# Kernel tuning notes

Measured on AMD Instinct MI355X. Metric: run time of the kernel, lower is better.

The kernel has to match this reference:

```python
import jax, jax.numpy as jnp
import numpy as np

B, T, L, H = 16, 16, 512, 768


def setup_inputs() -> dict:
    key = jax.random.key(0)
    k1, k2, k3, k4, k5, k6 = jax.random.split(key, 6)
    hn = jax.random.normal(k1, (B, L, H), dtype=jnp.float32)
    decoder_out = jax.random.normal(k2, (B, L, H), dtype=jnp.float32)
    W1 = jax.random.normal(k3, (H, H), dtype=jnp.float32) * (1.0 / np.sqrt(H))
    W2 = jax.random.normal(k4, (H, H), dtype=jnp.float32) * (1.0 / np.sqrt(H))
    V = jax.random.normal(k5, (H,), dtype=jnp.float32) * (1.0 / np.sqrt(H))
    # Ragged, consistent pointer indices: T monotone segment starts per sample,
    # gold boundary Yindex[b,t] in [Xindex[b,t], L).
    step = L // T  # 32
    Xindex = jnp.broadcast_to(jnp.arange(T, dtype=jnp.int64) * step, (B, T))
    offsets = jax.random.randint(k6, (B, T), 0, step, dtype=jnp.int64)
    Yindex = Xindex + offsets
    lens = jnp.full((B,), L, dtype=jnp.int64)
    return {"hn": hn, "decoder_out": decoder_out, "W1": W1, "W2": W2, "V": V,
            "Xindex": Xindex, "Yindex": Yindex, "lens": lens}


def reference(hn, decoder_out, W1, W2, V, Xindex, Yindex, lens):
    # Faithful batched form of training_decoder + pointerLayer:
    #   for each sample i, step j:
    #     en = hn[i, Xindex[i,j]:lens[i]]            (ragged suffix)
    #     dj = decoder_out[i, Yindex[i,j]]           (cur_dj = decoder_out[cur_groundy])
    #     s  = selu(V @ selu(W1 en + W2 dj))
    #     loss += NLL(log_softmax(s), Yindex[i,j]-Xindex[i,j])
    WE = jnp.einsum('blh,gh->blg', hn, W1)                        # [B,L,H]  nnW1(en)
    dj = jnp.take_along_axis(decoder_out, Yindex[:, :, None], axis=1)  # [B,T,H]
    WD = jnp.einsum('bth,gh->btg', dj, W2)                        # [B,T,H]  nnW2(dj)
    act = jax.nn.selu(WE[:, None, :, :] + WD[:, :, None, :])      # [B,T,L,H]
    scores = jax.nn.selu(jnp.einsum('btlh,h->btl', act, V))       # [B,T,L]
    pos = jnp.arange(hn.shape[1])
    mask = (pos[None, None, :] >= Xindex[:, :, None]) & (pos[None, None, :] < lens[:, None, None])
    neg_inf = jnp.finfo(scores.dtype).min
    masked = jnp.where(mask, scores, neg_inf)
    logp = masked - jax.scipy.special.logsumexp(masked, axis=-1, keepdims=True)
    # logits index (Yindex - Xindex) in the sliced array == global index Yindex
    gold = jnp.take_along_axis(logp, Yindex[:, :, None], axis=-1)[..., 0]  # [B,T]
    return -jnp.mean(gold)
```

## Files before the change

### kernel.cpp

```cpp
#include <hip/hip_runtime.h>
#include <hip/hip_bf16.h>
#include <math.h>

#define SELU_SCALE 1.0507009873554805f
#define SELU_ALPHA 1.6732632423543772f

static constexpr int B_ = 16, T_ = 16, L_ = 512, H_ = 768;

typedef __bf16 bf16x8 __attribute__((ext_vector_type(8)));
typedef __bf16 bf16x4 __attribute__((ext_vector_type(4)));
typedef float  f32x4  __attribute__((ext_vector_type(4)));

__device__ __forceinline__ float bf_lo(unsigned u) { return __uint_as_float(u << 16); }
__device__ __forceinline__ float bf_hi(unsigned u) { return __uint_as_float(u & 0xFFFF0000u); }

__device__ __forceinline__ float selu_core(float x) {
    float e = fmaf(__expf(x), SELU_ALPHA, -SELU_ALPHA);
    return x > 0.0f ? x : e;
}

__device__ __forceinline__ bf16x4 cvt4(float4 f) {
    bf16x4 o;
    o.x = (__bf16)f.x; o.y = (__bf16)f.y; o.z = (__bf16)f.z; o.w = (__bf16)f.w;
    return o;
}

__device__ __forceinline__ int xsw(int r) { return (r >> 1) & 3; }

__global__ __launch_bounds__(256) void prep_k(
        const float* __restrict__ w1, const float* __restrict__ w2,
        const float* __restrict__ dec, const int* __restrict__ Yi,
        __bf16* __restrict__ w1b, __bf16* __restrict__ w2b,
        float* __restrict__ djf, float* __restrict__ out) {
    const int NW = H_ * H_ / 4;
    int i = blockIdx.x * 256 + threadIdx.x;
    if (i == 0) out[0] = 0.0f;
    if (i < NW) {
        ((bf16x4*)w1b)[i] = cvt4(((const float4*)w1)[i]);
    } else if (i < 2 * NW) {
        int j = i - NW;
        ((bf16x4*)w2b)[j] = cvt4(((const float4*)w2)[j]);
    } else {
        int j = i - 2 * NW;
        int bt = j / 192, c = j % 192;
        int b = bt >> 4;
        int y = Yi[bt];
        ((float4*)djf)[bt * 192 + c] = ((const float4*)dec)[(b * L_ + y) * 192 + c];
    }
}

__global__ __launch_bounds__(256) void gemm_k(
        const float* __restrict__ hn, const float* __restrict__ djf,
        const __bf16* __restrict__ w1b, const __bf16* __restrict__ w2b,
        __bf16* __restrict__ web, __bf16* __restrict__ wdb) {
    __shared__ __bf16 As[64 * 32];
    __shared__ __bf16 Bs[128 * 32];

    int bx = blockIdx.x;
    const float* Af; const __bf16* Bw; __bf16* C; int m0, n0;
    if (bx < 768) {
        Af = hn;  Bw = w1b; C = web;
        m0 = (bx & 127) * 64; n0 = (bx >> 7) * 128;
    } else {
        bx -= 768;
        Af = djf; Bw = w2b; C = wdb;
        m0 = (bx & 3) * 64;   n0 = (bx >> 2) * 128;
    }

    const int tid = threadIdx.x;
    const int wave = tid >> 6, lane = tid & 63;
    const int wm = (wave >> 1) * 32, wn = (wave & 1) * 64;
    const int lr = lane & 15, q = lane >> 4;

    const int arow = tid >> 2, aseg = tid & 3;
    const float* Ag = Af + (size_t)(m0 + arow) * 768 + aseg * 8;
    bf16x8* AsW = (bf16x8*)&As[arow * 32 + ((aseg ^ xsw(arow)) * 8)];

    const int brow = tid >> 1, bs0 = (tid & 1) * 2;
    const __bf16* Bg = Bw + (size_t)(n0 + brow) * 768 + bs0 * 8;
    uint4* BsW0 = (uint4*)&Bs[brow * 32 + (((bs0)     ^ xsw(brow)) * 8)];
    uint4* BsW1 = (uint4*)&Bs[brow * 32 + (((bs0 + 1) ^ xsw(brow)) * 8)];

    int aoff[2], boff[4];
#pragma unroll
    for (int i = 0; i < 2; ++i) {
        int r = wm + i * 16 + lr;
        aoff[i] = r * 32 + (q ^ xsw(r)) * 8;
    }
#pragma unroll
    for (int j = 0; j < 4; ++j) {
        int r = wn + j * 16 + lr;
        boff[j] = r * 32 + (q ^ xsw(r)) * 8;
    }

    f32x4 acc[2][4] = {};

    float4 pax0 = *(const float4*)(Ag);      float4 pax1 = *(const float4*)(Ag + 4);
    uint4  pbx0 = *(const uint4*)(Bg);       uint4  pbx1 = *(const uint4*)(Bg + 8);
    float4 pay0 = *(const float4*)(Ag + 32); float4 pay1 = *(const float4*)(Ag + 36);
    uint4  pby0 = *(const uint4*)(Bg + 32);  uint4  pby1 = *(const uint4*)(Bg + 40);

#pragma unroll 1
    for (int k0 = 0; k0 < 768; k0 += 64) {
        {
            bf16x8 aw;
            aw[0] = (__bf16)pax0.x; aw[1] = (__bf16)pax0.y;
            aw[2] = (__bf16)pax0.z; aw[3] = (__bf16)pax0.w;
            aw[4] = (__bf16)pax1.x; aw[5] = (__bf16)pax1.y;
            aw[6] = (__bf16)pax1.z; aw[7] = (__bf16)pax1.w;
            *AsW  = aw;
            *BsW0 = pbx0;
            *BsW1 = pbx1;
            asm volatile("s_waitcnt lgkmcnt(0)\n\ts_barrier" ::: "memory");
            if (k0 + 64 < 768) {
                pax0 = *(const float4*)(Ag + k0 + 64);
                pax1 = *(const float4*)(Ag + k0 + 68);
                pbx0 = *(const uint4*)(Bg + k0 + 64);
                pbx1 = *(const uint4*)(Bg + k0 + 72);
            }
            bf16x8 af[2], bfr[4];
#pragma unroll
            for (int i = 0; i < 2; ++i) af[i]  = *(const bf16x8*)&As[aoff[i]];
#pragma unroll
            for (int j = 0; j < 4; ++j) bfr[j] = *(const bf16x8*)&Bs[boff[j]];
#pragma unroll
            for (int i = 0; i < 2; ++i)
#pragma unroll
                for (int j = 0; j < 4; ++j)
                    acc[i][j] = __builtin_amdgcn_mfma_f32_16x16x32_bf16(af[i], bfr[j], acc[i][j], 0, 0, 0);
            asm volatile("s_barrier" ::: "memory");
        }
        {
            bf16x8 aw;
            aw[0] = (__bf16)pay0.x; aw[1] = (__bf16)pay0.y;
            aw[2] = (__bf16)pay0.z; aw[3] = (__bf16)pay0.w;
            aw[4] = (__bf16)pay1.x; aw[5] = (__bf16)pay1.y;
            aw[6] = (__bf16)pay1.z; aw[7] = (__bf16)pay1.w;
            *AsW  = aw;
            *BsW0 = pby0;
            *BsW1 = pby1;
            asm volatile("s_waitcnt lgkmcnt(0)\n\ts_barrier" ::: "memory");
            if (k0 + 96 < 768) {
                pay0 = *(const float4*)(Ag + k0 + 96);
                pay1 = *(const float4*)(Ag + k0 + 100);
                pby0 = *(const uint4*)(Bg + k0 + 96);
                pby1 = *(const uint4*)(Bg + k0 + 104);
            }
            bf16x8 af[2], bfr[4];
#pragma unroll
            for (int i = 0; i < 2; ++i) af[i]  = *(const bf16x8*)&As[aoff[i]];
#pragma unroll
            for (int j = 0; j < 4; ++j) bfr[j] = *(const bf16x8*)&Bs[boff[j]];
#pragma unroll
            for (int i = 0; i < 2; ++i)
#pragma unroll
                for (int j = 0; j < 4; ++j)
                    acc[i][j] = __builtin_amdgcn_mfma_f32_16x16x32_bf16(af[i], bfr[j], acc[i][j], 0, 0, 0);
            asm volatile("s_barrier" ::: "memory");
        }
    }

#pragma unroll
    for (int i = 0; i < 2; ++i)
#pragma unroll
        for (int j = 0; j < 4; ++j)
#pragma unroll
            for (int r = 0; r < 4; ++r) {
                int row = m0 + wm + i * 16 + q * 4 + r;
                int col = n0 + wn + j * 16 + lr;
                C[(size_t)row * 768 + col] = (__bf16)acc[i][j][r];
            }
}

__global__ __launch_bounds__(256) void scores_k(
        const __bf16* __restrict__ web, const __bf16* __restrict__ wdb,
        const float* __restrict__ V, const int* __restrict__ Xi,
        float* __restrict__ scores) {
    __shared__ float    we_s[16][772];
    __shared__ unsigned wd_s[16][388];
    __shared__ float    v_s[768];

    const int b = blockIdx.x, l0 = blockIdx.y * 16;

    for (int c = threadIdx.x; c < 16 * 96; c += 256) {
        int r = c / 96, cc = c % 96;
        uint4 v = *(const uint4*)(web + ((size_t)(b * L_ + l0 + r)) * H_ + cc * 8);
        float4 f0, f1;
        f0.x = bf_lo(v.x); f0.y = bf_hi(v.x); f0.z = bf_lo(v.y); f0.w = bf_hi(v.y);
        f1.x = bf_lo(v.z); f1.y = bf_hi(v.z); f1.z = bf_lo(v.w); f1.w = bf_hi(v.w);
        *(float4*)&we_s[r][cc * 8]     = f0;
        *(float4*)&we_s[r][cc * 8 + 4] = f1;
    }
    for (int c = threadIdx.x; c < 16 * 96; c += 256) {
        int r = c / 96, cc = c % 96;
        *(uint4*)&wd_s[r][cc * 4] = *(const uint4*)(wdb + ((size_t)(b * T_ + r)) * H_ + cc * 8);
    }
    if (threadIdx.x < 192) *(float4*)&v_s[threadIdx.x * 4] = ((const float4*)V)[threadIdx.x];
    __syncthreads();

    const int t = threadIdx.x >> 4;
    const int ls = threadIdx.x & 15;
    const int l = l0 + ls;
    const int X = Xi[b * T_ + t];
    if (!__any(l >= X)) return;

    float a0 = 0.f, a1 = 0.f, a2 = 0.f, a3 = 0.f;
#pragma unroll 4
    for (int h = 0; h < H_; h += 8) {
        float4 w0 = *(const float4*)&we_s[ls][h];
        float4 w1 = *(const float4*)&we_s[ls][h + 4];
        uint4  wd = *(const uint4*)&wd_s[t][h >> 1];
        float4 v0 = *(const float4*)&v_s[h];
        float4 v1 = *(const float4*)&v_s[h + 4];
        a0 = fmaf(selu_core(w0.x + bf_lo(wd.x)), v0.x, a0);
        a1 = fmaf(selu_core(w0.y + bf_hi(wd.x)), v0.y, a1);
        a2 = fmaf(selu_core(w0.z + bf_lo(wd.y)), v0.z, a2);
        a3 = fmaf(selu_core(w0.w + bf_hi(wd.y)), v0.w, a3);
        a0 = fmaf(selu_core(w1.x + bf_lo(wd.z)), v1.x, a0);
        a1 = fmaf(selu_core(w1.y + bf_hi(wd.z)), v1.y, a1);
        a2 = fmaf(selu_core(w1.z + bf_lo(wd.w)), v1.z, a2);
        a3 = fmaf(selu_core(w1.w + bf_hi(wd.w)), v1.w, a3);
    }
    float dot = SELU_SCALE * ((a0 + a1) + (a2 + a3));
    float sc  = dot > 0.0f ? SELU_SCALE * dot
                           : SELU_SCALE * SELU_ALPHA * (__expf(dot) - 1.0f);
    scores[((size_t)(b * T_ + t)) * L_ + l] = sc;
}

__global__ __launch_bounds__(64) void loss_k(
        const float* __restrict__ scores, const int* __restrict__ Xi,
        const int* __restrict__ Yi, float* __restrict__ out) {
    const int bt = blockIdx.x;
    const int lane = threadIdx.x;
    const int X = Xi[bt];
    const int Y = Yi[bt];
    const float* row = scores + (size_t)bt * L_;

    float m = -INFINITY;
    for (int l = X + lane; l < L_; l += 64) m = fmaxf(m, row[l]);
#pragma unroll
    for (int off = 32; off > 0; off >>= 1) m = fmaxf(m, __shfl_xor(m, off));

    float s = 0.0f;
    for (int l = X + lane; l < L_; l += 64) s += __expf(row[l] - m);
#pragma unroll
    for (int off = 32; off > 0; off >>= 1) s += __shfl_xor(s, off);

    if (lane == 0)
        atomicAdd(out, (m + __logf(s) - row[Y]) * (1.0f / (B_ * T_)));
}

extern "C" void kernel_launch(void* const* d_in, const int* in_sizes, int n_in,
                              void* d_out, int out_size, void* d_ws, size_t ws_size,
                              hipStream_t stream) {
    const float* hn  = (const float*)d_in[0];
    const float* dec = (const float*)d_in[1];
    const float* W1  = (const float*)d_in[2];
    const float* W2  = (const float*)d_in[3];
    const float* V   = (const float*)d_in[4];
    const int*   Xi  = (const int*)d_in[5];
    const int*   Yi  = (const int*)d_in[6];
    float* out = (float*)d_out;

    char* ws = (char*)d_ws;
    size_t off = 0;
    auto alloc = [&](size_t bytes) -> char* {
        char* p = ws + off;
        off += (bytes + 255) & ~(size_t)255;
        return p;
    };
    __bf16* w1b    = (__bf16*)alloc((size_t)H_ * H_ * 2);
    __bf16* w2b    = (__bf16*)alloc((size_t)H_ * H_ * 2);
    float*  djf    = (float*)alloc((size_t)B_ * T_ * H_ * 4);
    __bf16* web    = (__bf16*)alloc((size_t)B_ * L_ * H_ * 2);
    __bf16* wdb    = (__bf16*)alloc((size_t)B_ * T_ * H_ * 2);
    float*  scores = (float*)alloc((size_t)B_ * T_ * L_ * 4);

    prep_k<<<1344, 256, 0, stream>>>(W1, W2, dec, Yi, w1b, w2b, djf, out);
    gemm_k<<<792, 256, 0, stream>>>(hn, djf, w1b, w2b, web, wdb);
    scores_k<<<dim3(B_, L_ / 16), 256, 0, stream>>>(web, wdb, V, Xi, scores);
    loss_k<<<B_ * T_, 64, 0, stream>>>(scores, Xi, Yi, out);
}
```

Measured before the change: 158.6 us.

## Use 512-thread blocks in GEMM with 8 waves each owning a 32x32 tile

The projection GEMM moves from 256 to 512 threads per block, so eight waves each compute a 32x32 sub-tile instead of four waves computing 32x64. The same 64x128 block tile now spreads its B-tile loads over all threads, and A-tile loads are done only by the first 256 threads. The goal is more waves per CU to hide memory latency and fewer registers per thread, at the cost of less MFMA work per LDS read and more barrier participants.

```diff
diff --git a/kernel.cpp b/kernel.cpp
--- a/kernel.cpp
+++ b/kernel.cpp
@@ -49,7 +49,7 @@
     }
 }
 
-__global__ __launch_bounds__(256) void gemm_k(
+__global__ __launch_bounds__(512) void gemm_k(
         const float* __restrict__ hn, const float* __restrict__ djf,
         const __bf16* __restrict__ w1b, const __bf16* __restrict__ w2b,
         __bf16* __restrict__ web, __bf16* __restrict__ wdb) {
@@ -69,92 +69,99 @@
 
     const int tid = threadIdx.x;
     const int wave = tid >> 6, lane = tid & 63;
-    const int wm = (wave >> 1) * 32, wn = (wave & 1) * 64;
+    const int wm = (wave >> 2) * 32, wn = (wave & 3) * 32;
     const int lr = lane & 15, q = lane >> 4;
 
-    const int arow = tid >> 2, aseg = tid & 3;
+    const bool doA = (tid < 256);
+    const int arow = (tid & 255) >> 2, aseg = tid & 3;
     const float* Ag = Af + (size_t)(m0 + arow) * 768 + aseg * 8;
     bf16x8* AsW = (bf16x8*)&As[arow * 32 + ((aseg ^ xsw(arow)) * 8)];
 
-    const int brow = tid >> 1, bs0 = (tid & 1) * 2;
-    const __bf16* Bg = Bw + (size_t)(n0 + brow) * 768 + bs0 * 8;
-    uint4* BsW0 = (uint4*)&Bs[brow * 32 + (((bs0)     ^ xsw(brow)) * 8)];
-    uint4* BsW1 = (uint4*)&Bs[brow * 32 + (((bs0 + 1) ^ xsw(brow)) * 8)];
-
-    int aoff[2], boff[4];
+    const int brow = tid >> 2, bseg = tid & 3;
+    const __bf16* Bg = Bw + (size_t)(n0 + brow) * 768 + bseg * 8;
+    uint4* BsW = (uint4*)&Bs[brow * 32 + ((bseg ^ xsw(brow)) * 8)];
+
+    int aoff[2], boff[2];
 #pragma unroll
     for (int i = 0; i < 2; ++i) {
         int r = wm + i * 16 + lr;
         aoff[i] = r * 32 + (q ^ xsw(r)) * 8;
     }
 #pragma unroll
-    for (int j = 0; j < 4; ++j) {
+    for (int j = 0; j < 2; ++j) {
         int r = wn + j * 16 + lr;
         boff[j] = r * 32 + (q ^ xsw(r)) * 8;
     }
 
-    f32x4 acc[2][4] = {};
-
-    float4 pax0 = *(const float4*)(Ag);      float4 pax1 = *(const float4*)(Ag + 4);
-    uint4  pbx0 = *(const uint4*)(Bg);       uint4  pbx1 = *(const uint4*)(Bg + 8);
-    float4 pay0 = *(const float4*)(Ag + 32); float4 pay1 = *(const float4*)(Ag + 36);
-    uint4  pby0 = *(const uint4*)(Bg + 32);  uint4  pby1 = *(const uint4*)(Bg + 40);
+    f32x4 acc[2][2] = {};
+
+    float4 pax0{}, pax1{}, pay0{}, pay1{};
+    if (doA) {
+        pax0 = *(const float4*)(Ag);      pax1 = *(const float4*)(Ag + 4);
+        pay0 = *(const float4*)(Ag + 32); pay1 = *(const float4*)(Ag + 36);
+    }
+    uint4 pbx = *(const uint4*)(Bg);
+    uint4 pby = *(const uint4*)(Bg + 32);
 
 #pragma unroll 1
     for (int k0 = 0; k0 < 768; k0 += 64) {
         {
-            bf16x8 aw;
-            aw[0] = (__bf16)pax0.x; aw[1] = (__bf16)pax0.y;
-            aw[2] = (__bf16)pax0.z; aw[3] = (__bf16)pax0.w;
-            aw[4] = (__bf16)pax1.x; aw[5] = (__bf16)pax1.y;
-            aw[6] = (__bf16)pax1.z; aw[7] = (__bf16)pax1.w;
-            *AsW  = aw;
-            *BsW0 = pbx0;
-            *BsW1 = pbx1;
+            if (doA) {
+                bf16x8 aw;
+                aw[0] = (__bf16)pax0.x; aw[1] = (__bf16)pax0.y;
+                aw[2] = (__bf16)pax0.z; aw[3] = (__bf16)pax0.w;
+                aw[4] = (__bf16)pax1.x; aw[5] = (__bf16)pax1.y;
+                aw[6] = (__bf16)pax1.z; aw[7] = (__bf16)pax1.w;
+                *AsW = aw;
+            }
+            *BsW = pbx;
             asm volatile("s_waitcnt lgkmcnt(0)\n\ts_barrier" ::: "memory");
             if (k0 + 64 < 768) {
-                pax0 = *(const float4*)(Ag + k0 + 64);
-                pax1 = *(const float4*)(Ag + k0 + 68);
-                pbx0 = *(const uint4*)(Bg + k0 + 64);
-                pbx1 = *(const uint4*)(Bg + k0 + 72);
-            }
-            bf16x8 af[2], bfr[4];
+                if (doA) {
+                    pax0 = *(const float4*)(Ag + k0 + 64);
+                    pax1 = *(const float4*)(Ag + k0 + 68);
+                }
+                pbx = *(const uint4*)(Bg + k0 + 64);
+            }
+            bf16x8 af[2], bfr[2];
 #pragma unroll
             for (int i = 0; i < 2; ++i) af[i]  = *(const bf16x8*)&As[aoff[i]];
 #pragma unroll
-            for (int j = 0; j < 4; ++j) bfr[j] = *(const bf16x8*)&Bs[boff[j]];
+            for (int j = 0; j < 2; ++j) bfr[j] = *(const bf16x8*)&Bs[boff[j]];
 #pragma unroll
             for (int i = 0; i < 2; ++i)
 #pragma unroll
-                for (int j = 0; j < 4; ++j)
+                for (int j = 0; j < 2; ++j)
                     acc[i][j] = __builtin_amdgcn_mfma_f32_16x16x32_bf16(af[i], bfr[j], acc[i][j], 0, 0, 0);
             asm volatile("s_barrier" ::: "memory");
         }
         {
-            bf16x8 aw;
-            aw[0] = (__bf16)pay0.x; aw[1] = (__bf16)pay0.y;
-            aw[2] = (__bf16)pay0.z; aw[3] = (__bf16)pay0.w;
-            aw[4] = (__bf16)pay1.x; aw[5] = (__bf16)pay1.y;
-            aw[6] = (__bf16)pay1.z; aw[7] = (__bf16)pay1.w;
-            *AsW  = aw;
-            *BsW0 = pby0;
-            *BsW1 = pby1;
+            if (doA) {
+                bf16x8 aw;
+                aw[0] = (__bf16)pay0.x; aw[1] = (__bf16)pay0.y;
+                aw[2] = (__bf16)pay0.z; aw[3] = (__bf16)pay0.w;
+                aw[4] = (__bf16)pay1.x; aw[5] = (__bf16)pay1.y;
+                aw[6] = (__bf16)pay1.z; aw[7] = (__bf16)pay1.w;
+                *AsW = aw;
+            }
+            *BsW = pby;
             asm volatile("s_waitcnt lgkmcnt(0)\n\ts_barrier" ::: "memory");
             if (k0 + 96 < 768) {
-                pay0 = *(const float4*)(Ag + k0 + 96);
-                pay1 = *(const float4*)(Ag + k0 + 100);
-                pby0 = *(const uint4*)(Bg + k0 + 96);
-                pby1 = *(const uint4*)(Bg + k0 + 104);
-            }
-            bf16x8 af[2], bfr[4];
+                if (doA) {
+                    pay0 = *(const float4*)(Ag + k0 + 96);
+                    pay1 = *(const float4*)(Ag + k0 + 100);
+                }
+                pby = *(const uint4*)(Bg + k0 + 96);
+            }
+            bf16x8 af[2], bfr[2];
 #pragma unroll
             for (int i = 0; i < 2; ++i) af[i]  = *(const bf16x8*)&As[aoff[i]];
 #pragma unroll
-            for (int j = 0; j < 4; ++j) bfr[j] = *(const bf16x8*)&Bs[boff[j]];
+            for (int j = 0; j < 2; ++j) bfr[j] = *(const bf16x8*)&Bs[boff[j]];
 #pragma unroll
             for (int i = 0; i < 2; ++i)
 #pragma unroll
-                for (int j = 0; j < 4; ++j)
+                for (int j = 0; j < 2; ++j)
                     acc[i][j] = __builtin_amdgcn_mfma_f32_16x16x32_bf16(af[i], bfr[j], acc[i][j], 0, 0, 0);
             asm volatile("s_barrier" ::: "memory");
         }
@@ -163,7 +170,7 @@
 #pragma unroll
     for (int i = 0; i < 2; ++i)
 #pragma unroll
-        for (int j = 0; j < 4; ++j)
+        for (int j = 0; j < 2; ++j)
 #pragma unroll
             for (int r = 0; r < 4; ++r) {
                 int row = m0 + wm + i * 16 + q * 4 + r;
@@ -277,7 +284,7 @@
     float*  scores = (float*)alloc((size_t)B_ * T_ * L_ * 4);
 
     prep_k<<<1344, 256, 0, stream>>>(W1, W2, dec, Yi, w1b, w2b, djf, out);
-    gemm_k<<<792, 256, 0, stream>>>(hn, djf, w1b, w2b, web, wdb);
+    gemm_k<<<792, 512, 0, stream>>>(hn, djf, w1b, w2b, web, wdb);
     scores_k<<<dim3(B_, L_ / 16), 256, 0, stream>>>(web, wdb, V, Xi, scores);
     loss_k<<<B_ * T_, 64, 0, stream>>>(scores, Xi, Yi, out);
 }
```

After: 157.0 us. No clear change (-1.1%).

## Fuse weight conversion and gather into GEMM, enlarge tile to 128x128

Applied to the files above, without the earlier changes.

The separate prep kernel is removed. The GEMM now reads fp32 W1/W2 directly and converts them to bf16 while staging into shared memory, and it gathers decoder rows by Yindex inline. The M tile grows from 64 to 128, so each wave holds a 4x4 block of MFMA accumulators, and the grid halves to 396 blocks with a launch_bounds occupancy hint. This saves one launch and the round trip through the intermediate buffers, but the weights are now converted redundantly by every block, more fp32 bytes are loaded per tile, and fewer blocks may leave CUs underused.

```diff
diff --git a/kernel.cpp b/kernel.cpp
--- a/kernel.cpp
+++ b/kernel.cpp
@@ -8,7 +8,6 @@
 static constexpr int B_ = 16, T_ = 16, L_ = 512, H_ = 768;
 
 typedef __bf16 bf16x8 __attribute__((ext_vector_type(8)));
-typedef __bf16 bf16x4 __attribute__((ext_vector_type(4)));
 typedef float  f32x4  __attribute__((ext_vector_type(4)));
 
 __device__ __forceinline__ float bf_lo(unsigned u) { return __uint_as_float(u << 16); }
@@ -19,71 +18,65 @@
     return x > 0.0f ? x : e;
 }
 
-__device__ __forceinline__ bf16x4 cvt4(float4 f) {
-    bf16x4 o;
-    o.x = (__bf16)f.x; o.y = (__bf16)f.y; o.z = (__bf16)f.z; o.w = (__bf16)f.w;
+__device__ __forceinline__ int xsw(int r) { return (r >> 1) & 3; }
+
+__device__ __forceinline__ bf16x8 pack8(float4 a, float4 b) {
+    bf16x8 o;
+    o[0] = (__bf16)a.x; o[1] = (__bf16)a.y; o[2] = (__bf16)a.z; o[3] = (__bf16)a.w;
+    o[4] = (__bf16)b.x; o[5] = (__bf16)b.y; o[6] = (__bf16)b.z; o[7] = (__bf16)b.w;
     return o;
 }
 
-__device__ __forceinline__ int xsw(int r) { return (r >> 1) & 3; }
-
-__global__ __launch_bounds__(256) void prep_k(
+__global__ __launch_bounds__(256, 2) void gemm_k(
+        const float* __restrict__ hn, const float* __restrict__ dec,
         const float* __restrict__ w1, const float* __restrict__ w2,
-        const float* __restrict__ dec, const int* __restrict__ Yi,
-        __bf16* __restrict__ w1b, __bf16* __restrict__ w2b,
-        float* __restrict__ djf, float* __restrict__ out) {
-    const int NW = H_ * H_ / 4;
-    int i = blockIdx.x * 256 + threadIdx.x;
-    if (i == 0) out[0] = 0.0f;
-    if (i < NW) {
-        ((bf16x4*)w1b)[i] = cvt4(((const float4*)w1)[i]);
-    } else if (i < 2 * NW) {
-        int j = i - NW;
-        ((bf16x4*)w2b)[j] = cvt4(((const float4*)w2)[j]);
+        const int* __restrict__ Yi,
+        __bf16* __restrict__ web, __bf16* __restrict__ wdb,
+        float* __restrict__ out) {
+    __shared__ __bf16 As[128 * 32];
+    __shared__ __bf16 Bs[128 * 32];
+
+    const int tid = threadIdx.x;
+    if (blockIdx.x == 0 && tid == 0) out[0] = 0.0f;
+
+    int bx = blockIdx.x;
+    const float* Wf; __bf16* C; int m0, n0; bool wd;
+    if (bx < 384) {
+        wd = false; Wf = w1; C = web;
+        m0 = (bx & 63) * 128; n0 = (bx >> 6) * 128;
     } else {
-        int j = i - 2 * NW;
-        int bt = j / 192, c = j % 192;
-        int b = bt >> 4;
-        int y = Yi[bt];
-        ((float4*)djf)[bt * 192 + c] = ((const float4*)dec)[(b * L_ + y) * 192 + c];
-    }
-}
-
-__global__ __launch_bounds__(256) void gemm_k(
-        const float* __restrict__ hn, const float* __restrict__ djf,
-        const __bf16* __restrict__ w1b, const __bf16* __restrict__ w2b,
-        __bf16* __restrict__ web, __bf16* __restrict__ wdb) {
-    __shared__ __bf16 As[64 * 32];
-    __shared__ __bf16 Bs[128 * 32];
-
-    int bx = blockIdx.x;
-    const float* Af; const __bf16* Bw; __bf16* C; int m0, n0;
-    if (bx < 768) {
-        Af = hn;  Bw = w1b; C = web;
-        m0 = (bx & 127) * 64; n0 = (bx >> 7) * 128;
+        wd = true; bx -= 384; Wf = w2; C = wdb;
+        m0 = (bx & 1) * 128;  n0 = (bx >> 1) * 128;
+    }
+
+    const int wave = tid >> 6, lane = tid & 63;
+    const int wm = (wave >> 1) * 64, wn = (wave & 1) * 64;
+    const int lr = lane & 15, q = lane >> 4;
+
+    const int r1 = wave * 32 + (lane >> 2);
+    const int s3 = lane & 3;
+    const int g1 = s3 ^ xsw(r1);
+
+    const float *aG1, *aG2;
+    if (!wd) {
+        aG1 = hn + (size_t)(m0 + r1) * 768 + g1 * 8;
+        aG2 = aG1 + (size_t)16 * 768;
     } else {
-        bx -= 768;
-        Af = djf; Bw = w2b; C = wdb;
-        m0 = (bx & 3) * 64;   n0 = (bx >> 2) * 128;
-    }
-
-    const int tid = threadIdx.x;
-    const int wave = tid >> 6, lane = tid & 63;
-    const int wm = (wave >> 1) * 32, wn = (wave & 1) * 64;
-    const int lr = lane & 15, q = lane >> 4;
-
-    const int arow = tid >> 2, aseg = tid & 3;
-    const float* Ag = Af + (size_t)(m0 + arow) * 768 + aseg * 8;
-    bf16x8* AsW = (bf16x8*)&As[arow * 32 + ((aseg ^ xsw(arow)) * 8)];
-
-    const int brow = tid >> 1, bs0 = (tid & 1) * 2;
-    const __bf16* Bg = Bw + (size_t)(n0 + brow) * 768 + bs0 * 8;
-    uint4* BsW0 = (uint4*)&Bs[brow * 32 + (((bs0)     ^ xsw(brow)) * 8)];
-    uint4* BsW1 = (uint4*)&Bs[brow * 32 + (((bs0 + 1) ^ xsw(brow)) * 8)];
-
-    int aoff[2], boff[4];
-#pragma unroll
-    for (int i = 0; i < 2; ++i) {
+        int bt1 = m0 + r1, bt2 = bt1 + 16;
+        aG1 = dec + ((size_t)((bt1 >> 4) * L_ + Yi[bt1])) * 768 + g1 * 8;
+        aG2 = dec + ((size_t)((bt2 >> 4) * L_ + Yi[bt2])) * 768 + g1 * 8;
+    }
+    const float* bG1 = Wf + (size_t)(n0 + r1) * 768 + g1 * 8;
+    const float* bG2 = bG1 + (size_t)16 * 768;
+
+    bf16x8* AsW1 = (bf16x8*)&As[r1 * 32 + s3 * 8];
+    bf16x8* AsW2 = (bf16x8*)&As[(r1 + 16) * 32 + s3 * 8];
+    bf16x8* BsW1 = (bf16x8*)&Bs[r1 * 32 + s3 * 8];
+    bf16x8* BsW2 = (bf16x8*)&Bs[(r1 + 16) * 32 + s3 * 8];
+
+    int aoff[4], boff[4];
+#pragma unroll
+    for (int i = 0; i < 4; ++i) {
         int r = wm + i * 16 + lr;
         aoff[i] = r * 32 + (q ^ xsw(r)) * 8;
     }
@@ -93,66 +86,62 @@
         boff[j] = r * 32 + (q ^ xsw(r)) * 8;
     }
 
-    f32x4 acc[2][4] = {};
-
-    float4 pax0 = *(const float4*)(Ag);      float4 pax1 = *(const float4*)(Ag + 4);
-    uint4  pbx0 = *(const uint4*)(Bg);       uint4  pbx1 = *(const uint4*)(Bg + 8);
-    float4 pay0 = *(const float4*)(Ag + 32); float4 pay1 = *(const float4*)(Ag + 36);
-    uint4  pby0 = *(const uint4*)(Bg + 32);  uint4  pby1 = *(const uint4*)(Bg + 40);
+    f32x4 acc[4][4] = {};
+
+    float4 xa1a = *(const float4*)(aG1);      float4 xa1b = *(const float4*)(aG1 + 4);
+    float4 xa2a = *(const float4*)(aG2);      float4 xa2b = *(const float4*)(aG2 + 4);
+    float4 xb1a = *(const float4*)(bG1);      float4 xb1b = *(const float4*)(bG1 + 4);
+    float4 xb2a = *(const float4*)(bG2);      float4 xb2b = *(const float4*)(bG2 + 4);
+    float4 ya1a = *(const float4*)(aG1 + 32); float4 ya1b = *(const float4*)(aG1 + 36);
+    float4 ya2a = *(const float4*)(aG2 + 32); float4 ya2b = *(const float4*)(aG2 + 36);
+    float4 yb1a = *(const float4*)(bG1 + 32); float4 yb1b = *(const float4*)(bG1 + 36);
+    float4 yb2a = *(const float4*)(bG2 + 32); float4 yb2b = *(const float4*)(bG2 + 36);
 
 #pragma unroll 1
     for (int k0 = 0; k0 < 768; k0 += 64) {
         {
-            bf16x8 aw;
-            aw[0] = (__bf16)pax0.x; aw[1] = (__bf16)pax0.y;
-            aw[2] = (__bf16)pax0.z; aw[3] = (__bf16)pax0.w;
-            aw[4] = (__bf16)pax1.x; aw[5] = (__bf16)pax1.y;
-            aw[6] = (__bf16)pax1.z; aw[7] = (__bf16)pax1.w;
-            *AsW  = aw;
-            *BsW0 = pbx0;
-            *BsW1 = pbx1;
+            *AsW1 = pack8(xa1a, xa1b);
+            *AsW2 = pack8(xa2a, xa2b);
+            *BsW1 = pack8(xb1a, xb1b);
+            *BsW2 = pack8(xb2a, xb2b);
             asm volatile("s_waitcnt lgkmcnt(0)\n\ts_barrier" ::: "memory");
             if (k0 + 64 < 768) {
-                pax0 = *(const float4*)(Ag + k0 + 64);
-                pax1 = *(const float4*)(Ag + k0 + 68);
-                pbx0 = *(const uint4*)(Bg + k0 + 64);
-                pbx1 = *(const uint4*)(Bg + k0 + 72);
+                xa1a = *(const float4*)(aG1 + k0 + 64); xa1b = *(const float4*)(aG1 + k0 + 68);
+                xa2a = *(const float4*)(aG2 + k0 + 64); xa2b = *(const float4*)(aG2 + k0 + 68);
+                xb1a = *(const float4*)(bG1 + k0 + 64); xb1b = *(const float4*)(bG1 + k0 + 68);
+                xb2a = *(const float4*)(bG2 + k0 + 64); xb2b = *(const float4*)(bG2 + k0 + 68);
             }
-            bf16x8 af[2], bfr[4];
-#pragma unroll
-            for (int i = 0; i < 2; ++i) af[i]  = *(const bf16x8*)&As[aoff[i]];
+            bf16x8 af[4], bfr[4];
+#pragma unroll
+            for (int i = 0; i < 4; ++i) af[i]  = *(const bf16x8*)&As[aoff[i]];
 #pragma unroll
             for (int j = 0; j < 4; ++j) bfr[j] = *(const bf16x8*)&Bs[boff[j]];
 #pragma unroll
-            for (int i = 0; i < 2; ++i)
+            for (int i = 0; i < 4; ++i)
 #pragma unroll
                 for (int j = 0; j < 4; ++j)
                     acc[i][j] = __builtin_amdgcn_mfma_f32_16x16x32_bf16(af[i], bfr[j], acc[i][j], 0, 0, 0);
             asm volatile("s_barrier" ::: "memory");
         }
         {
-            bf16x8 aw;
-            aw[0] = (__bf16)pay0.x; aw[1] = (__bf16)pay0.y;
-            aw[2] = (__bf16)pay0.z; aw[3] = (__bf16)pay0.w;
-            aw[4] = (__bf16)pay1.x; aw[5] = (__bf16)pay1.y;
-            aw[6] = (__bf16)pay1.z; aw[7] = (__bf16)pay1.w;
-            *AsW  = aw;
-            *BsW0 = pby0;
-            *BsW1 = pby1;
+            *AsW1 = pack8(ya1a, ya1b);
+            *AsW2 = pack8(ya2a, ya2b);
+            *BsW1 = pack8(yb1a, yb1b);
+            *BsW2 = pack8(yb2a, yb2b);
             asm volatile("s_waitcnt lgkmcnt(0)\n\ts_barrier" ::: "memory");
             if (k0 + 96 < 768) {
-                pay0 = *(const float4*)(Ag + k0 + 96);
-                pay1 = *(const float4*)(Ag + k0 + 100);
-                pby0 = *(const uint4*)(Bg + k0 + 96);
-                pby1 = *(const uint4*)(Bg + k0 + 104);
+                ya1a = *(const float4*)(aG1 + k0 + 96); ya1b = *(const float4*)(aG1 + k0 + 100);
+                ya2a = *(const float4*)(aG2 + k0 + 96); ya2b = *(const float4*)(aG2 + k0 + 100);
+                yb1a = *(const float4*)(bG1 + k0 + 96); yb1b = *(const float4*)(bG1 + k0 + 100);
+                yb2a = *(const float4*)(bG2 + k0 + 96); yb2b = *(const float4*)(bG2 + k0 + 100);
             }
-            bf16x8 af[2], bfr[4];
-#pragma unroll
-            for (int i = 0; i < 2; ++i) af[i]  = *(const bf16x8*)&As[aoff[i]];
+            bf16x8 af[4], bfr[4];
+#pragma unroll
+            for (int i = 0; i < 4; ++i) af[i]  = *(const bf16x8*)&As[aoff[i]];
 #pragma unroll
             for (int j = 0; j < 4; ++j) bfr[j] = *(const bf16x8*)&Bs[boff[j]];
 #pragma unroll
-            for (int i = 0; i < 2; ++i)
+            for (int i = 0; i < 4; ++i)
 #pragma unroll
                 for (int j = 0; j < 4; ++j)
                     acc[i][j] = __builtin_amdgcn_mfma_f32_16x16x32_bf16(af[i], bfr[j], acc[i][j], 0, 0, 0);
@@ -161,7 +150,7 @@
     }
 
 #pragma unroll
-    for (int i = 0; i < 2; ++i)
+    for (int i = 0; i < 4; ++i)
 #pragma unroll
         for (int j = 0; j < 4; ++j)
 #pragma unroll
@@ -269,15 +258,11 @@
         off += (bytes + 255) & ~(size_t)255;
         return p;
     };
-    __bf16* w1b    = (__bf16*)alloc((size_t)H_ * H_ * 2);
-    __bf16* w2b    = (__bf16*)alloc((size_t)H_ * H_ * 2);
-    float*  djf    = (float*)alloc((size_t)B_ * T_ * H_ * 4);
     __bf16* web    = (__bf16*)alloc((size_t)B_ * L_ * H_ * 2);
     __bf16* wdb    = (__bf16*)alloc((size_t)B_ * T_ * H_ * 2);
     float*  scores = (float*)alloc((size_t)B_ * T_ * L_ * 4);
 
-    prep_k<<<1344, 256, 0, stream>>>(W1, W2, dec, Yi, w1b, w2b, djf, out);
-    gemm_k<<<792, 256, 0, stream>>>(hn, djf, w1b, w2b, web, wdb);
+    gemm_k<<<396, 256, 0, stream>>>(hn, dec, W1, W2, Yi, web, wdb, out);
     scores_k<<<dim3(B_, L_ / 16), 256, 0, stream>>>(web, wdb, V, Xi, scores);
     loss_k<<<B_ * T_, 64, 0, stream>>>(scores, Xi, Yi, out);
 }
```

After: 152.4 us. -3.9%, faster.
